# Performance work log

Hardware: AMD Instinct MI355X
Metric: run time of the kernel (lower is better)

The kernel has to match this reference:

```python
import jax, jax.numpy as jnp
import numpy as np
import math

D_MODEL = 1024
N_HEADS = 16
HEAD_DIM = D_MODEL // N_HEADS
SEQ = 2048
BATCH = 4
MAX_SEQ_LEN = 2048
THETA = 10000.0


def setup_inputs() -> dict:
    key = jax.random.key(0)
    ks = jax.random.split(key, 5)
    std = math.sqrt(2.0 / (D_MODEL + D_MODEL))
    x = jax.random.normal(ks[0], (BATCH, SEQ, D_MODEL), dtype=jnp.float32)
    wq = jax.random.normal(ks[1], (D_MODEL, D_MODEL), dtype=jnp.float32) * std
    wk = jax.random.normal(ks[2], (D_MODEL, D_MODEL), dtype=jnp.float32) * std
    wv = jax.random.normal(ks[3], (D_MODEL, D_MODEL), dtype=jnp.float32) * std
    wo = jax.random.normal(ks[4], (D_MODEL, D_MODEL), dtype=jnp.float32) * std
    token_positions = jnp.arange(SEQ, dtype=jnp.int32)
    return {"x": x, "token_positions": token_positions,
            "wq": wq, "wk": wk, "wv": wv, "wo": wo}


def _rope_tables(token_positions):
    # thetas_i = 1 / theta^(2i/d_k), angles[p, i] = p * thetas_i
    thetas = 1.0 / (THETA ** (2.0 * jnp.arange(HEAD_DIM // 2, dtype=jnp.float32) / HEAD_DIM))
    positions = jnp.arange(MAX_SEQ_LEN, dtype=jnp.float32)
    angles = jnp.outer(positions, thetas)  # [max_seq, d_k/2]
    cos = jnp.cos(angles)[token_positions]  # [S, d_k/2]
    sin = jnp.sin(angles)[token_positions]
    return cos, sin


def _apply_rope(x, cos, sin):
    # x: [B, H, S, D]; pairs (even, odd) form complex numbers
    shp = x.shape
    x2 = x.reshape(*shp[:-1], HEAD_DIM // 2, 2)
    xe, xo = x2[..., 0], x2[..., 1]
    re = xe * cos - xo * sin
    im = xe * sin + xo * cos
    return jnp.stack([re, im], axis=-1).reshape(shp)


def reference(x, token_positions, wq, wk, wv, wo):
    B, S, _ = x.shape
    # LinearNoBias: einsum('...j,ij->...i', x, W)
    q = jnp.einsum('bsj,ij->bsi', x, wq)
    k = jnp.einsum('bsj,ij->bsi', x, wk)
    v = jnp.einsum('bsj,ij->bsi', x, wv)
    # split heads -> [B, H, S, D]
    q = q.reshape(B, S, N_HEADS, HEAD_DIM).transpose(0, 2, 1, 3)
    k = k.reshape(B, S, N_HEADS, HEAD_DIM).transpose(0, 2, 1, 3)
    v = v.reshape(B, S, N_HEADS, HEAD_DIM).transpose(0, 2, 1, 3)
    cos, sin = _rope_tables(token_positions)
    q = _apply_rope(q, cos, sin)
    k = _apply_rope(k, cos, sin)
    scores = jnp.einsum('bhqd,bhkd->bhqk', q, k) / math.sqrt(HEAD_DIM)
    causal = jnp.tril(jnp.ones((S, S), dtype=bool))
    scores = jnp.where(causal, scores, -jnp.inf)
    probs = jax.nn.softmax(scores, axis=-1)
    out = jnp.einsum('bhqk,bhkd->bhqd', probs, v)
    out = out.transpose(0, 2, 1, 3).reshape(B, S, N_HEADS * HEAD_DIM)
    return jnp.einsum('bsj,ij->bsi', out, wo)
```

## Files before the change

kernel.cpp:

```cpp
#include <hip/hip_runtime.h>
#include <stdint.h>

#define B_SZ 4
#define S_LEN 2048
#define NH 16
#define HD 64
#define DM 1024

typedef __bf16 bf16;
typedef __bf16 bf16x4 __attribute__((ext_vector_type(4)));
typedef __bf16 bf16x8 __attribute__((ext_vector_type(8)));
typedef float f32x4 __attribute__((ext_vector_type(4)));

#define MFMA16(a, b, c) __builtin_amdgcn_mfma_f32_16x16x32_bf16(a, b, c, 0, 0, 0)

__device__ __forceinline__ void gl2lds16(const void* g, void* l) {
  __builtin_amdgcn_global_load_lds(
      (__attribute__((address_space(1))) const void*)g,
      (__attribute__((address_space(3))) void*)l, 16, 0, 0);
}

__device__ __forceinline__ bf16x8 ldcvt(const float* p) {
  f32x4 u0 = *(const f32x4*)p;
  f32x4 u1 = *(const f32x4*)(p + 4);
  bf16x8 v;
#pragma unroll
  for (int j = 0; j < 4; j++) {
    v[j] = (bf16)u0[j];
    v[4 + j] = (bf16)u1[j];
  }
  return v;
}

__global__ void cvt_kernel(const float* __restrict__ x,
                           const float* __restrict__ wq,
                           const float* __restrict__ wk,
                           const float* __restrict__ wv,
                           const float* __restrict__ wo,
                           bf16* __restrict__ Xb, bf16* __restrict__ Wb,
                           long xN) {
  const long e = ((long)blockIdx.x * 256 + threadIdx.x) * 8;
  const float* src;
  bf16* dst;
  long off;
  if (e < xN) {
    src = x; dst = Xb; off = e;
  } else {
    const long w = e - xN;
    const int wi = (int)(w >> 20);
    src = (wi == 0) ? wq : (wi == 1) ? wk : (wi == 2) ? wv : wo;
    dst = Wb + ((size_t)wi << 20);
    off = w & ((1L << 20) - 1);
  }
  *(bf16x8*)(dst + off) = ldcvt(src + off);
}

__device__ __forceinline__ void gemm_core_bb(const bf16* __restrict__ Ag,
                                             const bf16* __restrict__ Bg,
                                             f32x4 acc[4][4], bf16* As,
                                             bf16* Bs) {
  const int tid = threadIdx.x;
  const int lane = tid & 63;
  const int wave = tid >> 6;
  const int wm = (wave >> 1) * 64;
  const int wn = (wave & 1) * 64;
  const int col = lane & 15;
  const int kq = (lane >> 4) * 8;
  const int r0 = tid >> 2;
  const int c0 = (tid & 3) * 8;
#pragma unroll
  for (int i = 0; i < 4; i++)
#pragma unroll
    for (int j = 0; j < 4; j++) acc[i][j] = (f32x4){0.f, 0.f, 0.f, 0.f};

  for (int k0 = 0; k0 < 1024; k0 += 32) {
    __syncthreads();
    gl2lds16(Ag + (size_t)r0 * 1024 + k0 + c0, As + tid * 8);
    gl2lds16(Ag + (size_t)(r0 + 64) * 1024 + k0 + c0, As + 2048 + tid * 8);
    gl2lds16(Bg + (size_t)r0 * 1024 + k0 + c0, Bs + tid * 8);
    gl2lds16(Bg + (size_t)(r0 + 64) * 1024 + k0 + c0, Bs + 2048 + tid * 8);
    __syncthreads();

    bf16x8 af[4], bfr[4];
#pragma unroll
    for (int i = 0; i < 4; i++)
      af[i] = *(const bf16x8*)(As + (wm + i * 16 + col) * 32 + kq);
#pragma unroll
    for (int j = 0; j < 4; j++)
      bfr[j] = *(const bf16x8*)(Bs + (wn + j * 16 + col) * 32 + kq);
#pragma unroll
    for (int i = 0; i < 4; i++)
#pragma unroll
      for (int j = 0; j < 4; j++)
        acc[i][j] = MFMA16(af[i], bfr[j], acc[i][j]);
  }
}

__global__ __launch_bounds__(256, 4) void qkv_gemm(
    const bf16* __restrict__ x, const bf16* __restrict__ Wb,
    bf16* __restrict__ Q, bf16* __restrict__ K, bf16* __restrict__ Vt) {
  __shared__ __align__(16) bf16 As[128 * 32];
  __shared__ __align__(16) bf16 Bs[128 * 32];
  const int bx = blockIdx.x;
  const int by = blockIdx.y;
  const int wsel = by >> 3;
  const int n0 = (by & 7) * 128;

  f32x4 acc[4][4];
  gemm_core_bb(x + (size_t)bx * 128 * 1024,
               Wb + ((size_t)wsel << 20) + (size_t)n0 * 1024, acc, As, Bs);

  const int lane = threadIdx.x & 63;
  const int wave = threadIdx.x >> 6;
  const int wm = (wave >> 1) * 64, wn = (wave & 1) * 64;
  const int col = lane & 15, quad = lane >> 4;

  if (wsel < 2) {
    bf16* dst = wsel ? K : Q;
#pragma unroll
    for (int i = 0; i < 4; i++) {
      const int m0 = bx * 128 + wm + i * 16 + quad * 4;
#pragma unroll
      for (int j = 0; j < 4; j++) {
        const int n = n0 + wn + j * 16 + col;
        const int h = n >> 6, d = n & 63;
#pragma unroll
        for (int r = 0; r < 4; r++) {
          const int mm = m0 + r;
          const int bl = mm >> 11, s = mm & 2047;
          dst[((((size_t)bl * NH + h) * S_LEN + s) << 6) + d] =
              (bf16)acc[i][j][r];
        }
      }
    }
  } else {
#pragma unroll
    for (int i = 0; i < 4; i++) {
      const int m0 = bx * 128 + wm + i * 16 + quad * 4;
      const int bl = m0 >> 11, s = m0 & 2047;
#pragma unroll
      for (int j = 0; j < 4; j++) {
        const int n = n0 + wn + j * 16 + col;
        const int h = n >> 6, d = n & 63;
        bf16x4 pk;
#pragma unroll
        for (int r = 0; r < 4; r++) pk[r] = (bf16)acc[i][j][r];
        *(bf16x4*)(Vt + (((size_t)(bl * NH + h) * 64 + d) << 11) + s) = pk;
      }
    }
  }
}

__global__ void rope_kernel(bf16* __restrict__ q, bf16* __restrict__ k,
                            const int* __restrict__ tp) {
  const float CS = 0.18033688011112042f;
  const int idx = blockIdx.x * 256 + threadIdx.x;
  const int srow = idx >> 3;
  const int d0 = (idx & 7) * 8;
  const int s = srow & (S_LEN - 1);
  const float pf = (float)tp[s];
  const int i0 = d0 >> 1;
  float cs[4], sn[4];
#pragma unroll
  for (int j = 0; j < 4; j++) {
    float freq = __builtin_exp2f(-(float)(i0 + j) * 0.41524101186091903f);
    float ang = pf * freq;
    sincosf(ang, &sn[j], &cs[j]);
  }
  const size_t off = (size_t)srow * 64 + d0;
  bf16x8 vq = *(bf16x8*)(q + off);
  bf16x8 vk = *(bf16x8*)(k + off);
#pragma unroll
  for (int j = 0; j < 4; j++) {
    float e = (float)vq[2 * j], o = (float)vq[2 * j + 1];
    vq[2 * j] = (bf16)((e * cs[j] - o * sn[j]) * CS);
    vq[2 * j + 1] = (bf16)((e * sn[j] + o * cs[j]) * CS);
    e = (float)vk[2 * j];
    o = (float)vk[2 * j + 1];
    vk[2 * j] = (bf16)(e * cs[j] - o * sn[j]);
    vk[2 * j + 1] = (bf16)(e * sn[j] + o * cs[j]);
  }
  *(bf16x8*)(q + off) = vq;
  *(bf16x8*)(k + off) = vk;
}

#define KP 72
#define VP 136
#define PP 72
__global__ __launch_bounds__(256, 2) void attn_kernel(
    const bf16* __restrict__ Q, const bf16* __restrict__ K,
    const bf16* __restrict__ Vt, bf16* __restrict__ O) {
  __shared__ __align__(16) bf16 Ks[128 * KP];
  __shared__ __align__(16) bf16 Vts[64 * VP];
  __shared__ __align__(16) bf16 Ps[4 * 64 * PP];

  const int tid = threadIdx.x, lane = tid & 63, wave = tid >> 6;
  const int col = lane & 15, quad = lane >> 4, kq = quad * 8;
  const int bh = blockIdx.y;
  const int qt = (blockIdx.y >= (gridDim.y >> 1)) ? (int)blockIdx.x
                                                  : 7 - (int)blockIdx.x;
  const int bl = bh >> 4, h = bh & 15;
  const bf16* Kg = K + (size_t)bh * S_LEN * 64;
  const bf16* Vg = Vt + (size_t)bh * 64 * S_LEN;
  bf16* Pw = Ps + wave * 64 * PP;
  const int wq0 = wave * 64;
  const int qbase = qt * 256;
  const int qmax = qbase + wq0 + 63;

  const bf16* Qg = Q + ((size_t)bh * S_LEN + qbase) * 64;
  bf16x8 qf[4][2];
#pragma unroll
  for (int mi = 0; mi < 4; mi++)
#pragma unroll
    for (int kc = 0; kc < 2; kc++)
      qf[mi][kc] =
          *(const bf16x8*)(Qg + (wq0 + mi * 16 + col) * 64 + kc * 32 + kq);

  f32x4 oacc[4][4];
  float lst[4] = {0.f, 0.f, 0.f, 0.f};
#pragma unroll
  for (int mi = 0; mi < 4; mi++)
#pragma unroll
    for (int nd = 0; nd < 4; nd++) oacc[mi][nd] = (f32x4){0.f, 0.f, 0.f, 0.f};

  const int kiters = 2 * qt + 2;
  for (int kt = 0; kt < kiters; kt++) {
    bf16x8 kreg[4], vreg[4];
#pragma unroll
    for (int p = 0; p < 4; p++) {
      int g = p * 256 + tid;
      kreg[p] = *(const bf16x8*)(Kg + (size_t)(kt * 128 + (g >> 3)) * 64 +
                                 (g & 7) * 8);
      vreg[p] = *(const bf16x8*)(Vg + (size_t)(g >> 4) * S_LEN + kt * 128 +
                                 (g & 15) * 8);
    }
    __syncthreads();
#pragma unroll
    for (int p = 0; p < 4; p++) {
      int g = p * 256 + tid;
      *(bf16x8*)(Ks + (g >> 3) * KP + (g & 7) * 8) = kreg[p];
      *(bf16x8*)(Vts + (g >> 4) * VP + (g & 15) * 8) = vreg[p];
    }
    __syncthreads();
    if (kt * 128 > qmax) continue;

#pragma unroll
    for (int hf = 0; hf < 2; hf++) {
      const int kb = kt * 128 + hf * 64;
      if (kb > qmax) break;
      f32x4 sa[4][4];
#pragma unroll
      for (int ni = 0; ni < 4; ni++) {
        const int krow = hf * 64 + ni * 16 + col;
        bf16x8 kf0 = *(const bf16x8*)(Ks + krow * KP + kq);
        bf16x8 kf1 = *(const bf16x8*)(Ks + krow * KP + 32 + kq);
#pragma unroll
        for (int mi = 0; mi < 4; mi++) {
          f32x4 s = {0.f, 0.f, 0.f, 0.f};
          s = MFMA16(kf0, qf[mi][0], s);
          s = MFMA16(kf1, qf[mi][1], s);
          sa[mi][ni] = s;
        }
      }
      if (kb + 63 > qbase + wq0) {
        const int base = kb - qbase - wq0 + quad * 4;
#pragma unroll
        for (int mi = 0; mi < 4; mi++)
#pragma unroll
          for (int ni = 0; ni < 4; ni++)
#pragma unroll
            for (int r = 0; r < 4; r++)
              if (base + ni * 16 + r > mi * 16 + col) sa[mi][ni][r] = -1e30f;
      }
#pragma unroll
      for (int mi = 0; mi < 4; mi++) {
        float rs = 0.f;
#pragma unroll
        for (int ni = 0; ni < 4; ni++)
#pragma unroll
          for (int r = 0; r < 4; r++) {
            float pv = __builtin_exp2f(sa[mi][ni][r]);
            sa[mi][ni][r] = pv;
            rs += pv;
          }
        lst[mi] += rs;
      }
#pragma unroll
      for (int mi = 0; mi < 4; mi++)
#pragma unroll
        for (int ni = 0; ni < 4; ni++) {
          bf16x4 pk;
#pragma unroll
          for (int r = 0; r < 4; r++) pk[r] = (bf16)sa[mi][ni][r];
          *(bf16x4*)(Pw + (mi * 16 + col) * PP + ni * 16 + quad * 4) = pk;
        }
#pragma unroll
      for (int kcl = 0; kcl < 2; kcl++) {
        bf16x8 pf[4];
#pragma unroll
        for (int mi = 0; mi < 4; mi++)
          pf[mi] = *(const bf16x8*)(Pw + (mi * 16 + col) * PP + kcl * 32 + kq);
#pragma unroll
        for (int nd = 0; nd < 4; nd++) {
          bf16x8 vf = *(const bf16x8*)(Vts + (nd * 16 + col) * VP + hf * 64 +
                                       kcl * 32 + kq);
#pragma unroll
          for (int mi = 0; mi < 4; mi++)
            oacc[mi][nd] = MFMA16(pf[mi], vf, oacc[mi][nd]);
        }
      }
    }
  }

#pragma unroll
  for (int mi = 0; mi < 4; mi++) {
    float rs = lst[mi];
    rs += __shfl_xor(rs, 16);
    rs += __shfl_xor(rs, 32);
    const float il = 1.0f / rs;
    float linv[4];
#pragma unroll
    for (int r = 0; r < 4; r++) linv[r] = __shfl(il, quad * 4 + r);
    const int srow0 = qbase + wq0 + mi * 16 + quad * 4;
#pragma unroll
    for (int nd = 0; nd < 4; nd++)
#pragma unroll
      for (int r = 0; r < 4; r++)
        O[(size_t)(bl * S_LEN + srow0 + r) * DM + h * 64 + nd * 16 + col] =
            (bf16)(oacc[mi][nd][r] * linv[r]);
  }
}

__global__ __launch_bounds__(256, 4) void out_gemm(const bf16* __restrict__ A,
                                                   const bf16* __restrict__ W,
                                                   float* __restrict__ out) {
  __shared__ __align__(16) bf16 As[128 * 32];
  __shared__ __align__(16) bf16 Bs[128 * 32];
  f32x4 acc[4][4];
  gemm_core_bb(A + (size_t)blockIdx.x * 128 * 1024,
               W + (size_t)blockIdx.y * 128 * 1024, acc, As, Bs);
  const int lane = threadIdx.x & 63;
  const int wave = threadIdx.x >> 6;
  const int wm = (wave >> 1) * 64, wn = (wave & 1) * 64;
  const int col = lane & 15, quad = lane >> 4;
#pragma unroll
  for (int i = 0; i < 4; i++) {
    const int m0 = blockIdx.x * 128 + wm + i * 16 + quad * 4;
#pragma unroll
    for (int j = 0; j < 4; j++) {
      const int n = blockIdx.y * 128 + wn + j * 16 + col;
#pragma unroll
      for (int r = 0; r < 4; r++)
        out[(size_t)(m0 + r) * DM + n] = acc[i][j][r];
    }
  }
}

extern "C" void kernel_launch(void* const* d_in, const int* in_sizes, int n_in,
                              void* d_out, int out_size, void* d_ws,
                              size_t ws_size, hipStream_t stream) {
  const float* x = (const float*)d_in[0];
  const int* tp = (const int*)d_in[1];
  const float* wq = (const float*)d_in[2];
  const float* wk = (const float*)d_in[3];
  const float* wv = (const float*)d_in[4];
  const float* wo = (const float*)d_in[5];
  float* out = (float*)d_out;
  bf16* wsb = (bf16*)d_ws;

  const size_t TENb = (size_t)NH * S_LEN * HD;
  const size_t WSZ = 4ull * DM * DM;
  int bcnt = 1;
  if (ws_size >= (4 * 4 * TENb + WSZ) * sizeof(bf16)) bcnt = 4;
  else if (ws_size >= (4 * 2 * TENb + WSZ) * sizeof(bf16)) bcnt = 2;

  const size_t REG = (size_t)bcnt * TENb;
  bf16* Xb = wsb;
  bf16* Qw = wsb + REG;
  bf16* Kw = wsb + 2 * REG;
  bf16* Vtw = wsb + 3 * REG;
  bf16* Wb = wsb + 4 * REG;
  bf16* Ow = Xb;

  for (int b0 = 0; b0 < B_SZ; b0 += bcnt) {
    const float* xb = x + (size_t)b0 * S_LEN * DM;
    float* outb = out + (size_t)b0 * S_LEN * DM;
    const long cvtN = (long)(REG + WSZ);
    hipLaunchKernelGGL(cvt_kernel, dim3((unsigned)(cvtN / 2048)), dim3(256), 0,
                       stream, xb, wq, wk, wv, wo, Xb, Wb, (long)REG);
    hipLaunchKernelGGL(qkv_gemm, dim3(bcnt * 16, 24), dim3(256), 0, stream,
                       Xb, Wb, Qw, Kw, Vtw);
    hipLaunchKernelGGL(rope_kernel, dim3(bcnt * 1024), dim3(256), 0, stream,
                       Qw, Kw, tp);
    hipLaunchKernelGGL(attn_kernel, dim3(8, bcnt * 16), dim3(256), 0, stream,
                       Qw, Kw, Vtw, Ow);
    hipLaunchKernelGGL(out_gemm, dim3(bcnt * 16, 8), dim3(256), 0, stream,
                       Ow, Wb + 3ull * DM * DM, outb);
  }
}
```

Measured before the change: 280.4 us.

## Read K/V fragments directly from global memory in attention, drop LDS staging

The attention kernel no longer stages K and V tiles through shared memory with two block barriers per tile. Each wave now loads its MFMA fragments straight from global memory (relying on L1/L2 caching) and iterates only up to its own causal limit, so waves in a block are decoupled. The grid is transposed so that blocks with the same query tile but different heads launch together, with the heaviest tiles scheduled first. This removes barrier stalls and LDS traffic, but repeats global/L2 loads per wave and loses the coalesced cooperative loads.

```diff
diff --git a/kernel.cpp b/kernel.cpp
--- a/kernel.cpp
+++ b/kernel.cpp
@@ -184,37 +184,31 @@
   *(bf16x8*)(k + off) = vk;
 }
 
-#define KP 72
-#define VP 136
 #define PP 72
 __global__ __launch_bounds__(256, 2) void attn_kernel(
     const bf16* __restrict__ Q, const bf16* __restrict__ K,
     const bf16* __restrict__ Vt, bf16* __restrict__ O) {
-  __shared__ __align__(16) bf16 Ks[128 * KP];
-  __shared__ __align__(16) bf16 Vts[64 * VP];
   __shared__ __align__(16) bf16 Ps[4 * 64 * PP];
 
   const int tid = threadIdx.x, lane = tid & 63, wave = tid >> 6;
   const int col = lane & 15, quad = lane >> 4, kq = quad * 8;
-  const int bh = blockIdx.y;
-  const int qt = (blockIdx.y >= (gridDim.y >> 1)) ? (int)blockIdx.x
-                                                  : 7 - (int)blockIdx.x;
+  const int bh = blockIdx.x;
+  const int yb = blockIdx.y;
+  const int qt = (yb < 4) ? (7 - yb) : (yb - 4);
   const int bl = bh >> 4, h = bh & 15;
   const bf16* Kg = K + (size_t)bh * S_LEN * 64;
   const bf16* Vg = Vt + (size_t)bh * 64 * S_LEN;
   bf16* Pw = Ps + wave * 64 * PP;
-  const int wq0 = wave * 64;
-  const int qbase = qt * 256;
-  const int qmax = qbase + wq0 + 63;
-
-  const bf16* Qg = Q + ((size_t)bh * S_LEN + qbase) * 64;
+  const int wq_abs = qt * 256 + wave * 64;
+
+  const bf16* Qg = Q + ((size_t)bh * S_LEN + wq_abs) * 64;
   bf16x8 qf[4][2];
 #pragma unroll
   for (int mi = 0; mi < 4; mi++)
 #pragma unroll
     for (int kc = 0; kc < 2; kc++)
       qf[mi][kc] =
-          *(const bf16x8*)(Qg + (wq0 + mi * 16 + col) * 64 + kc * 32 + kq);
+          *(const bf16x8*)(Qg + (mi * 16 + col) * 64 + kc * 32 + kq);
 
   f32x4 oacc[4][4];
   float lst[4] = {0.f, 0.f, 0.f, 0.f};
@@ -223,91 +217,66 @@
 #pragma unroll
     for (int nd = 0; nd < 4; nd++) oacc[mi][nd] = (f32x4){0.f, 0.f, 0.f, 0.f};
 
-  const int kiters = 2 * qt + 2;
-  for (int kt = 0; kt < kiters; kt++) {
-    bf16x8 kreg[4], vreg[4];
-#pragma unroll
-    for (int p = 0; p < 4; p++) {
-      int g = p * 256 + tid;
-      kreg[p] = *(const bf16x8*)(Kg + (size_t)(kt * 128 + (g >> 3)) * 64 +
-                                 (g & 7) * 8);
-      vreg[p] = *(const bf16x8*)(Vg + (size_t)(g >> 4) * S_LEN + kt * 128 +
-                                 (g & 15) * 8);
-    }
-    __syncthreads();
-#pragma unroll
-    for (int p = 0; p < 4; p++) {
-      int g = p * 256 + tid;
-      *(bf16x8*)(Ks + (g >> 3) * KP + (g & 7) * 8) = kreg[p];
-      *(bf16x8*)(Vts + (g >> 4) * VP + (g & 15) * 8) = vreg[p];
-    }
-    __syncthreads();
-    if (kt * 128 > qmax) continue;
-
-#pragma unroll
-    for (int hf = 0; hf < 2; hf++) {
-      const int kb = kt * 128 + hf * 64;
-      if (kb > qmax) break;
-      f32x4 sa[4][4];
+  for (int kb = 0; kb <= wq_abs + 63; kb += 64) {
+    f32x4 sa[4][4];
+#pragma unroll
+    for (int ni = 0; ni < 4; ni++) {
+      const bf16* kr = Kg + (size_t)(kb + ni * 16 + col) * 64;
+      bf16x8 kf0 = *(const bf16x8*)(kr + kq);
+      bf16x8 kf1 = *(const bf16x8*)(kr + 32 + kq);
+#pragma unroll
+      for (int mi = 0; mi < 4; mi++) {
+        f32x4 s = {0.f, 0.f, 0.f, 0.f};
+        s = MFMA16(kf0, qf[mi][0], s);
+        s = MFMA16(kf1, qf[mi][1], s);
+        sa[mi][ni] = s;
+      }
+    }
+    if (kb + 63 > wq_abs) {
+      const int base = kb - wq_abs + quad * 4;
+#pragma unroll
+      for (int mi = 0; mi < 4; mi++)
+#pragma unroll
+        for (int ni = 0; ni < 4; ni++)
+#pragma unroll
+          for (int r = 0; r < 4; r++)
+            if (base + ni * 16 + r > mi * 16 + col) sa[mi][ni][r] = -1e30f;
+    }
+#pragma unroll
+    for (int mi = 0; mi < 4; mi++) {
+      float rs = 0.f;
+#pragma unroll
+      for (int ni = 0; ni < 4; ni++)
+#pragma unroll
+        for (int r = 0; r < 4; r++) {
+          float pv = __builtin_exp2f(sa[mi][ni][r]);
+          sa[mi][ni][r] = pv;
+          rs += pv;
+        }
+      lst[mi] += rs;
+    }
+#pragma unroll
+    for (int mi = 0; mi < 4; mi++)
 #pragma unroll
       for (int ni = 0; ni < 4; ni++) {
-        const int krow = hf * 64 + ni * 16 + col;
-        bf16x8 kf0 = *(const bf16x8*)(Ks + krow * KP + kq);
-        bf16x8 kf1 = *(const bf16x8*)(Ks + krow * KP + 32 + kq);
-#pragma unroll
-        for (int mi = 0; mi < 4; mi++) {
-          f32x4 s = {0.f, 0.f, 0.f, 0.f};
-          s = MFMA16(kf0, qf[mi][0], s);
-          s = MFMA16(kf1, qf[mi][1], s);
-          sa[mi][ni] = s;
-        }
-      }
-      if (kb + 63 > qbase + wq0) {
-        const int base = kb - qbase - wq0 + quad * 4;
+        bf16x4 pk;
+#pragma unroll
+        for (int r = 0; r < 4; r++) pk[r] = (bf16)sa[mi][ni][r];
+        *(bf16x4*)(Pw + (mi * 16 + col) * PP + ni * 16 + quad * 4) = pk;
+      }
+#pragma unroll
+    for (int kcl = 0; kcl < 2; kcl++) {
+      bf16x8 pf[4];
+#pragma unroll
+      for (int mi = 0; mi < 4; mi++)
+        pf[mi] = *(const bf16x8*)(Pw + (mi * 16 + col) * PP + kcl * 32 + kq);
+#pragma unroll
+      for (int nd = 0; nd < 4; nd++) {
+        bf16x8 vf = *(const bf16x8*)(Vg + (size_t)(nd * 16 + col) * S_LEN +
+                                     kb + kcl * 32 + kq);
 #pragma unroll
         for (int mi = 0; mi < 4; mi++)
-#pragma unroll
-          for (int ni = 0; ni < 4; ni++)
-#pragma unroll
-            for (int r = 0; r < 4; r++)
-              if (base + ni * 16 + r > mi * 16 + col) sa[mi][ni][r] = -1e30f;
-      }
-#pragma unroll
-      for (int mi = 0; mi < 4; mi++) {
-        float rs = 0.f;
-#pragma unroll
-        for (int ni = 0; ni < 4; ni++)
-#pragma unroll
-          for (int r = 0; r < 4; r++) {
-            float pv = __builtin_exp2f(sa[mi][ni][r]);
-            sa[mi][ni][r] = pv;
-            rs += pv;
-          }
-        lst[mi] += rs;
-      }
-#pragma unroll
-      for (int mi = 0; mi < 4; mi++)
-#pragma unroll
-        for (int ni = 0; ni < 4; ni++) {
-          bf16x4 pk;
-#pragma unroll
-          for (int r = 0; r < 4; r++) pk[r] = (bf16)sa[mi][ni][r];
-          *(bf16x4*)(Pw + (mi * 16 + col) * PP + ni * 16 + quad * 4) = pk;
-        }
-#pragma unroll
-      for (int kcl = 0; kcl < 2; kcl++) {
-        bf16x8 pf[4];
-#pragma unroll
-        for (int mi = 0; mi < 4; mi++)
-          pf[mi] = *(const bf16x8*)(Pw + (mi * 16 + col) * PP + kcl * 32 + kq);
-#pragma unroll
-        for (int nd = 0; nd < 4; nd++) {
-          bf16x8 vf = *(const bf16x8*)(Vts + (nd * 16 + col) * VP + hf * 64 +
-                                       kcl * 32 + kq);
-#pragma unroll
-          for (int mi = 0; mi < 4; mi++)
-            oacc[mi][nd] = MFMA16(pf[mi], vf, oacc[mi][nd]);
-        }
+          oacc[mi][nd] = MFMA16(pf[mi], vf, oacc[mi][nd]);
       }
     }
   }
@@ -321,7 +290,7 @@
     float linv[4];
 #pragma unroll
     for (int r = 0; r < 4; r++) linv[r] = __shfl(il, quad * 4 + r);
-    const int srow0 = qbase + wq0 + mi * 16 + quad * 4;
+    const int srow0 = wq_abs + mi * 16 + quad * 4;
 #pragma unroll
     for (int nd = 0; nd < 4; nd++)
 #pragma unroll
@@ -392,7 +361,7 @@
                        Xb, Wb, Qw, Kw, Vtw);
     hipLaunchKernelGGL(rope_kernel, dim3(bcnt * 1024), dim3(256), 0, stream,
                        Qw, Kw, tp);
-    hipLaunchKernelGGL(attn_kernel, dim3(8, bcnt * 16), dim3(256), 0, stream,
+    hipLaunchKernelGGL(attn_kernel, dim3(bcnt * 16, 8), dim3(256), 0, stream,
                        Qw, Kw, Vtw, Ow);
     hipLaunchKernelGGL(out_gemm, dim3(bcnt * 16, 8), dim3(256), 0, stream,
                        Ow, Wb + 3ull * DM * DM, outb);
```

New measurement: 296.6 us. +5.8%, slower.

## Prefetch next K/V tile into registers and reorder attention grid

Applied to the files above, without the earlier changes.

The attention loop now loads the next K/V tile from global memory into registers while the current tile is computed, so global latency overlaps with the MFMA work. The old pair of __syncthreads is replaced by a custom barrier that waits only on LDS counters. The grid is also transposed so that blockIdx.x indexes batch-head and blockIdx.y indexes the query tile, with heavy causal tiles scheduled first. The prefetch adds register pressure, and the lgkmcnt-only barrier relies on the global loads having finished before their values are stored to LDS, which the compiler has to guarantee.

```diff
diff --git a/kernel.cpp b/kernel.cpp
--- a/kernel.cpp
+++ b/kernel.cpp
@@ -18,6 +18,10 @@
   __builtin_amdgcn_global_load_lds(
       (__attribute__((address_space(1))) const void*)g,
       (__attribute__((address_space(3))) void*)l, 16, 0, 0);
+}
+
+__device__ __forceinline__ void bar_lgkm() {
+  asm volatile("s_waitcnt lgkmcnt(0)\n\ts_barrier" ::: "memory");
 }
 
 __device__ __forceinline__ bf16x8 ldcvt(const float* p) {
@@ -196,25 +200,24 @@
 
   const int tid = threadIdx.x, lane = tid & 63, wave = tid >> 6;
   const int col = lane & 15, quad = lane >> 4, kq = quad * 8;
-  const int bh = blockIdx.y;
-  const int qt = (blockIdx.y >= (gridDim.y >> 1)) ? (int)blockIdx.x
-                                                  : 7 - (int)blockIdx.x;
+  const int bh = blockIdx.x;
+  const int yb = blockIdx.y;
+  const int qt = (yb < 4) ? (7 - yb) : (yb - 4);
   const int bl = bh >> 4, h = bh & 15;
   const bf16* Kg = K + (size_t)bh * S_LEN * 64;
   const bf16* Vg = Vt + (size_t)bh * 64 * S_LEN;
   bf16* Pw = Ps + wave * 64 * PP;
-  const int wq0 = wave * 64;
-  const int qbase = qt * 256;
-  const int qmax = qbase + wq0 + 63;
-
-  const bf16* Qg = Q + ((size_t)bh * S_LEN + qbase) * 64;
+  const int wq_abs = qt * 256 + wave * 64;
+  const int qmax = wq_abs + 63;
+
+  const bf16* Qg = Q + ((size_t)bh * S_LEN + wq_abs) * 64;
   bf16x8 qf[4][2];
 #pragma unroll
   for (int mi = 0; mi < 4; mi++)
 #pragma unroll
     for (int kc = 0; kc < 2; kc++)
       qf[mi][kc] =
-          *(const bf16x8*)(Qg + (wq0 + mi * 16 + col) * 64 + kc * 32 + kq);
+          *(const bf16x8*)(Qg + (mi * 16 + col) * 64 + kc * 32 + kq);
 
   f32x4 oacc[4][4];
   float lst[4] = {0.f, 0.f, 0.f, 0.f};
@@ -224,24 +227,33 @@
     for (int nd = 0; nd < 4; nd++) oacc[mi][nd] = (f32x4){0.f, 0.f, 0.f, 0.f};
 
   const int kiters = 2 * qt + 2;
+  bf16x8 kreg[4], vreg[4];
+#pragma unroll
+  for (int p = 0; p < 4; p++) {
+    const int g = p * 256 + tid;
+    kreg[p] = *(const bf16x8*)(Kg + (size_t)(g >> 3) * 64 + (g & 7) * 8);
+    vreg[p] = *(const bf16x8*)(Vg + (size_t)(g >> 4) * S_LEN + (g & 15) * 8);
+  }
+
   for (int kt = 0; kt < kiters; kt++) {
-    bf16x8 kreg[4], vreg[4];
+    bar_lgkm();
 #pragma unroll
     for (int p = 0; p < 4; p++) {
-      int g = p * 256 + tid;
-      kreg[p] = *(const bf16x8*)(Kg + (size_t)(kt * 128 + (g >> 3)) * 64 +
-                                 (g & 7) * 8);
-      vreg[p] = *(const bf16x8*)(Vg + (size_t)(g >> 4) * S_LEN + kt * 128 +
-                                 (g & 15) * 8);
-    }
-    __syncthreads();
-#pragma unroll
-    for (int p = 0; p < 4; p++) {
-      int g = p * 256 + tid;
+      const int g = p * 256 + tid;
       *(bf16x8*)(Ks + (g >> 3) * KP + (g & 7) * 8) = kreg[p];
       *(bf16x8*)(Vts + (g >> 4) * VP + (g & 15) * 8) = vreg[p];
     }
-    __syncthreads();
+    if (kt + 1 < kiters) {
+#pragma unroll
+      for (int p = 0; p < 4; p++) {
+        const int g = p * 256 + tid;
+        kreg[p] = *(const bf16x8*)(Kg + (size_t)((kt + 1) * 128 + (g >> 3)) * 64 +
+                                   (g & 7) * 8);
+        vreg[p] = *(const bf16x8*)(Vg + (size_t)(g >> 4) * S_LEN +
+                                   (kt + 1) * 128 + (g & 15) * 8);
+      }
+    }
+    bar_lgkm();
     if (kt * 128 > qmax) continue;
 
 #pragma unroll
@@ -262,8 +274,8 @@
           sa[mi][ni] = s;
         }
       }
-      if (kb + 63 > qbase + wq0) {
-        const int base = kb - qbase - wq0 + quad * 4;
+      if (kb + 63 > wq_abs) {
+        const int base = kb - wq_abs + quad * 4;
 #pragma unroll
         for (int mi = 0; mi < 4; mi++)
 #pragma unroll
@@ -321,7 +333,7 @@
     float linv[4];
 #pragma unroll
     for (int r = 0; r < 4; r++) linv[r] = __shfl(il, quad * 4 + r);
-    const int srow0 = qbase + wq0 + mi * 16 + quad * 4;
+    const int srow0 = wq_abs + mi * 16 + quad * 4;
 #pragma unroll
     for (int nd = 0; nd < 4; nd++)
 #pragma unroll
@@ -392,7 +404,7 @@
                        Xb, Wb, Qw, Kw, Vtw);
     hipLaunchKernelGGL(rope_kernel, dim3(bcnt * 1024), dim3(256), 0, stream,
                        Qw, Kw, tp);
-    hipLaunchKernelGGL(attn_kernel, dim3(8, bcnt * 16), dim3(256), 0, stream,
+    hipLaunchKernelGGL(attn_kernel, dim3(bcnt * 16, 8), dim3(256), 0, stream,
                        Qw, Kw, Vtw, Ow);
     hipLaunchKernelGGL(out_gemm, dim3(bcnt * 16, 8), dim3(256), 0, stream,
                        Ow, Wb + 3ull * DM * DM, outb);
```

After: 276.8 us. No clear change (-1.3%).
